# Kernel optimization log

Measured on AMD Instinct MI355X. Metric: run time of the kernel, lower is better.

Reference implementation:

```python
import jax, jax.numpy as jnp
import numpy as np

L, B, T, F, C, H, DFF = 2, 4, 2048, 1024, 200, 8, 128


def setup_inputs() -> dict:
    key = jax.random.key(0)
    ks = jax.random.split(key, 12)
    s = 0.02
    return {
        "x": jax.random.normal(ks[0], (B, T, F), jnp.float32),
        "prototypes": jax.random.normal(ks[1], (C, 1, F), jnp.float32),
        # conv_query / conv_key (1x1 convs == linear), per RAB layer
        "wq": jax.random.normal(ks[2], (L, F, F), jnp.float32) * s,
        "bq": jnp.zeros((L, F), jnp.float32),
        "wk": jax.random.normal(ks[3], (L, F, F), jnp.float32) * s,
        "bk": jnp.zeros((L, F), jnp.float32),
        # nn.MultiheadAttention packed in-proj and out-proj
        "in_w": jax.random.normal(ks[4], (L, 3 * F, F), jnp.float32) * s,
        "in_b": jnp.zeros((L, 3 * F), jnp.float32),
        "out_w": jax.random.normal(ks[5], (L, F, F), jnp.float32) * s,
        "out_b": jnp.zeros((L, F), jnp.float32),
        # FFN
        "l1_w": jax.random.normal(ks[6], (L, DFF, F), jnp.float32) * s,
        "l1_b": jnp.zeros((L, DFF), jnp.float32),
        "l2_w": jax.random.normal(ks[7], (L, F, DFF), jnp.float32) * s,
        "l2_b": jnp.zeros((L, F), jnp.float32),
        # LayerNorms
        "ln1_g": jnp.ones((L, F), jnp.float32),
        "ln1_b": jnp.zeros((L, F), jnp.float32),
        "ln2_g": jnp.ones((L, F), jnp.float32),
        "ln2_b": jnp.zeros((L, F), jnp.float32),
        # feature_embedding: Conv1d(F, F, k=3, pad=1) + ReLU
        "emb_w": jax.random.normal(ks[8], (F, F, 3), jnp.float32) * s,
        "emb_b": jnp.zeros((F,), jnp.float32),
    }


def _ln(x, g, b, eps=1e-5):
    mu = jnp.mean(x, axis=-1, keepdims=True)
    var = jnp.mean((x - mu) ** 2, axis=-1, keepdims=True)
    return (x - mu) * jax.lax.rsqrt(var + eps) * g + b


def _mha(q, k, v, w, b, ow, ob):
    # q,k,v: (B,S,F). Packed in-proj like nn.MultiheadAttention (eval: no dropout).
    f = q.shape[-1]
    dh = f // H
    Q = q @ w[:f].T + b[:f]
    K = k @ w[f:2 * f].T + b[f:2 * f]
    V = v @ w[2 * f:].T + b[2 * f:]
    sp = lambda t: t.reshape(t.shape[0], t.shape[1], H, dh)
    scale = np.float32(1.0 / np.sqrt(dh))
    att = jnp.einsum('bqhd,bkhd->bhqk', sp(Q), sp(K)) * scale
    att = jax.nn.softmax(att, axis=-1)
    o = jnp.einsum('bhqk,bkhd->bqhd', att, sp(V)).reshape(q.shape)
    return o @ ow.T + ob


def reference(x, prototypes, wq, bq, wk, bk, in_w, in_b, out_w, out_b,
              l1_w, l1_b, l2_w, l2_b, ln1_g, ln1_b, ln2_g, ln2_b, emb_w, emb_b):
    Bn, Tn, Fn = x.shape
    # torch: prototypes.view(1, F, -1)  (a reshape, NOT a transpose)
    proto = jnp.broadcast_to(prototypes.reshape(1, Fn, -1), (Bn, Fn, prototypes.shape[0]))
    # concat along time: (B,F,S) with S = T + C, then work in (B,S,F)
    src = jnp.swapaxes(jnp.concatenate([jnp.swapaxes(x, 1, 2), proto], axis=2), 1, 2)
    for l in range(L):
        q = src @ wq[l].T + bq[l]          # conv1x1 == pointwise linear
        k = src @ wk[l].T + bk[l]
        a = _mha(q, k, src, in_w[l], in_b[l], out_w[l], out_b[l])
        src = _ln(src + a, ln1_g[l], ln1_b[l])
        ff = jax.nn.relu(src @ l1_w[l].T + l1_b[l]) @ l2_w[l].T + l2_b[l]
        src = _ln(src + ff, ln2_g[l], ln2_b[l])
    feat = jnp.swapaxes(src[:, :Tn], 1, 2)  # (B,F,T): drop prototype tokens
    y = jax.lax.conv_general_dilated(feat, emb_w, (1,), ((1, 1),),
                                     dimension_numbers=('NCH', 'OIH', 'NCH'))
    return jax.nn.relu(y + emb_b[None, :, None])
```

## Files before the change

### kernel.cpp

```cpp
#include <hip/hip_runtime.h>
#include <hip/hip_bf16.h>


constexpr int BN = 4, TN = 2048, FD = 1024, CP = 200, SN = TN + CP;
constexpr int HN = 8, DH = 128, DF = 128, MR = BN * SN;
constexpr int SF = 3 * FD;
constexpr int NT = (SN + 63) / 64;
constexpr float C2 = 0.12751744f;

typedef __attribute__((ext_vector_type(8))) short short8;
typedef __attribute__((ext_vector_type(4))) float f32x4;

__device__ __forceinline__ ushort f2b(float f) {
  union { float f; uint u; } v{f};
  return (ushort)((v.u + 0x7fffu + ((v.u >> 16) & 1u)) >> 16);
}
__device__ __forceinline__ float b2f(ushort u) {
  union { uint u; float f; } v{(uint)u << 16};
  return v.f;
}
__device__ __forceinline__ uint cvt_pk_bf16(float a, float b) {
  uint r;
  asm("v_cvt_pk_bf16_f32 %0, %1, %2" : "=v"(r) : "v"(a), "v"(b));
  return r;
}
__device__ __forceinline__ float exp2_fast(float x) {
  float r;
  asm("v_exp_f32 %0, %1" : "=v"(r) : "v"(x));
  return r;
}
__device__ __forceinline__ void gld16(const void* g, void* l) {
  __builtin_amdgcn_global_load_lds(
      (const __attribute__((address_space(1))) void*)g,
      (__attribute__((address_space(3))) void*)l, 16, 0, 0);
}

__global__ __launch_bounds__(256) void k_build(const float* __restrict__ x,
                                               const float* __restrict__ proto,
                                               ushort* __restrict__ srcb) {
  const int row = blockIdx.x;
  const int b = row / SN, s = row % SN;
  const int f = threadIdx.x * 4;
  const size_t o = (size_t)row * FD + f;
  float4 v;
  if (s < TN) {
    v = *(const float4*)(x + ((size_t)b * TN + s) * FD + f);
  } else {
    const int c = s - TN;
    v.x = proto[(size_t)(f + 0) * CP + c];
    v.y = proto[(size_t)(f + 1) * CP + c];
    v.z = proto[(size_t)(f + 2) * CP + c];
    v.w = proto[(size_t)(f + 3) * CP + c];
  }
  ushort4 u{f2b(v.x), f2b(v.y), f2b(v.z), f2b(v.w)};
  *(ushort4*)(srcb + o) = u;
}

__global__ __launch_bounds__(256) void k_cvt(const float* __restrict__ in,
                                             ushort* __restrict__ out, int n) {
  const int n4 = n >> 2;
  for (int i = blockIdx.x * 256 + threadIdx.x; i < n4; i += gridDim.x * 256) {
    const float4 v = *(const float4*)(in + (size_t)i * 4);
    ushort4 u{f2b(v.x), f2b(v.y), f2b(v.z), f2b(v.w)};
    *(ushort4*)(out + (size_t)i * 4) = u;
  }
}

__global__ __launch_bounds__(256) void k_cvtT(const float* __restrict__ Wg,
                                              ushort* __restrict__ WTg) {
  const float* W = Wg + (size_t)blockIdx.z * FD * FD;
  ushort* WT = WTg + (size_t)blockIdx.z * FD * FD;
  __shared__ float t[32][33];
  const int tx = threadIdx.x & 31, ty = threadIdx.x >> 5;
  const int x0 = blockIdx.x * 32, y0 = blockIdx.y * 32;
#pragma unroll
  for (int dy = 0; dy < 4; ++dy)
    t[ty + dy * 8][tx] = W[(size_t)(y0 + ty + dy * 8) * FD + x0 + tx];
  __syncthreads();
#pragma unroll
  for (int dy = 0; dy < 4; ++dy)
    WT[(size_t)(x0 + ty + dy * 8) * FD + y0 + tx] = f2b(t[tx][ty + dy * 8]);
}

__global__ __launch_bounds__(256) void k_vT(const ushort* __restrict__ V,
                                            ushort* __restrict__ Vt) {
  __shared__ ushort t[32][34];
  const int tx = threadIdx.x & 31, ty = threadIdx.x >> 5;
  const int s0 = blockIdx.x * 32, d0 = blockIdx.y * 32, bh = blockIdx.z;
  const int b = bh >> 3, h = bh & 7;
#pragma unroll
  for (int dy = 0; dy < 4; ++dy) {
    const int s = min(s0 + ty + dy * 8, SN - 1);
    t[ty + dy * 8][tx] = V[((size_t)b * SN + s) * SF + h * DH + d0 + tx];
  }
  __syncthreads();
#pragma unroll
  for (int dy = 0; dy < 4; ++dy) {
    const int s = s0 + tx;
    if (s < SN)
      Vt[((size_t)bh * DH + d0 + ty + dy * 8) * SN + s] = t[tx][ty + dy * 8];
  }
}

__global__ __launch_bounds__(256) void k_convw(const float* __restrict__ W,
                                               ushort* __restrict__ out) {
  const int n = FD * FD * 3;
  for (int idx = blockIdx.x * 256 + threadIdx.x; idx < n;
       idx += gridDim.x * 256) {
    const int o = idx / (FD * 3);
    const int rem = idx % (FD * 3);
    const int tau = rem >> 10, i = rem & 1023;
    out[idx] = f2b(W[(size_t)o * (FD * 3) + i * 3 + tau]);
  }
}

__global__ __launch_bounds__(256) void k_pad(const ushort* __restrict__ sb,
                                             ushort* __restrict__ pad) {
  const int r = blockIdx.x, b = blockIdx.y;
  const int f = threadIdx.x * 4;
  ushort4 v{0, 0, 0, 0};
  if (r >= 1 && r <= TN)
    v = *(const ushort4*)(sb + ((size_t)b * SN + (r - 1)) * FD + f);
  *(ushort4*)(pad + ((size_t)b * (TN + 2) + r) * FD + f) = v;
}

__global__ __launch_bounds__(256) void k_beff(const float* __restrict__ in_w,
                                              const float* __restrict__ bvec,
                                              const float* __restrict__ in_b,
                                              float* __restrict__ out, int qk) {
  const int n = blockIdx.x, l = blockIdx.y, tid = threadIdx.x;
  const float* Win = in_w + (size_t)(l * 3 + qk) * FD * FD;
  const float* bv = bvec + (size_t)l * FD;
  float s = 0.f;
  for (int j = tid; j < FD; j += 256) s += Win[(size_t)n * FD + j] * bv[j];
  __shared__ float red[4];
#pragma unroll
  for (int o = 32; o; o >>= 1) s += __shfl_xor(s, o);
  if ((tid & 63) == 0) red[tid >> 6] = s;
  __syncthreads();
  if (tid == 0)
    out[l * 3 * FD + qk * FD + n] =
        red[0] + red[1] + red[2] + red[3] + in_b[l * 3 * FD + qk * FD + n];
}

__global__ __launch_bounds__(256) void k_copyv(const float* __restrict__ in_b,
                                               float* __restrict__ bqkv) {
  const int l = blockIdx.y;
  const int i = blockIdx.x * 256 + threadIdx.x;
  bqkv[l * 3 * FD + 2 * FD + i] = in_b[l * 3 * FD + 2 * FD + i];
}

template <bool RELU, bool BF16OUT>
__global__ __launch_bounds__(256) void k_mm(const ushort* __restrict__ A,
                                            const ushort* __restrict__ W,
                                            const float* __restrict__ bias,
                                            void* __restrict__ Cv,
                                            int M, int N, int K) {
  __shared__ __align__(16) ushort As[128 * 32];
  __shared__ __align__(16) ushort Ws[128 * 32];
  const int tid = threadIdx.x;
  const int lane = tid & 63, wv = tid >> 6;
  const int l15 = lane & 15, g = lane >> 4;
  const int wr = wv >> 1, wc = wv & 1;
  int bx = blockIdx.x, by = blockIdx.y;
  const int nwg = gridDim.x * gridDim.y;
  if ((nwg & 7) == 0) {
    int bid = by * gridDim.x + bx;
    bid = (bid & 7) * (nwg >> 3) + (bid >> 3);
    bx = bid % gridDim.x;
    by = bid / gridDim.x;
  }
  const int m0 = by * 128, n0 = bx * 128;
  f32x4 acc[4][4];
#pragma unroll
  for (int i = 0; i < 4; ++i)
#pragma unroll
    for (int j = 0; j < 4; ++j) acc[i][j] = (f32x4){0.f, 0.f, 0.f, 0.f};

  for (int k0 = 0; k0 < K; k0 += 32) {
#pragma unroll
    for (int j = 0; j < 2; ++j) {
      const int u = j * 256 + wv * 64 + lane;
      const int r = u >> 2, c = (u & 3) * 8;
      const int gm = min(m0 + r, M - 1);
      gld16(A + (size_t)gm * K + k0 + c, As + (size_t)u * 8);
    }
#pragma unroll
    for (int j = 0; j < 2; ++j) {
      const int u = j * 256 + wv * 64 + lane;
      const int r = u >> 2, c = (u & 3) * 8;
      gld16(W + (size_t)(n0 + r) * K + k0 + c, Ws + (size_t)u * 8);
    }
    __syncthreads();
    short8 af[4], bfr[4];
#pragma unroll
    for (int i = 0; i < 4; ++i)
      af[i] = *(const short8*)(As + (wr * 64 + i * 16 + l15) * 32 + g * 8);
#pragma unroll
    for (int j = 0; j < 4; ++j)
      bfr[j] = *(const short8*)(Ws + (wc * 64 + j * 16 + l15) * 32 + g * 8);
    __builtin_amdgcn_s_setprio(1);
#pragma unroll
    for (int i = 0; i < 4; ++i)
#pragma unroll
      for (int j = 0; j < 4; ++j)
        acc[i][j] = __builtin_amdgcn_mfma_f32_16x16x32_bf16(af[i], bfr[j],
                                                            acc[i][j], 0, 0, 0);
    __builtin_amdgcn_s_setprio(0);
    __syncthreads();
  }
#pragma unroll
  for (int i = 0; i < 4; ++i) {
#pragma unroll
    for (int r = 0; r < 4; ++r) {
      const int row = m0 + wr * 64 + i * 16 + g * 4 + r;
      if (row >= M) continue;
#pragma unroll
      for (int j = 0; j < 4; ++j) {
        const int col = n0 + wc * 64 + j * 16 + l15;
        float v = acc[i][j][r];
        if (bias) v += bias[col];
        if (RELU) v = fmaxf(v, 0.f);
        if (BF16OUT)
          ((ushort*)Cv)[(size_t)row * N + col] = f2b(v);
        else
          ((float*)Cv)[(size_t)row * N + col] = v;
      }
    }
  }
}

__global__ __launch_bounds__(256) void k_mmconv(const ushort* __restrict__ Ap,
                                                const ushort* __restrict__ W,
                                                const float* __restrict__ bias,
                                                float* __restrict__ Y) {
  constexpr int K = 3 * FD;
  __shared__ __align__(16) ushort As[128 * 32];
  __shared__ __align__(16) ushort Ws[128 * 32];
  const int tid = threadIdx.x;
  const int lane = tid & 63, wv = tid >> 6;
  const int l15 = lane & 15, g = lane >> 4;
  const int wr = wv >> 1, wc = wv & 1;
  int bx = blockIdx.x, by = blockIdx.y;
  const int nwg = gridDim.x * gridDim.y;
  if ((nwg & 7) == 0) {
    int bid = by * gridDim.x + bx;
    bid = (bid & 7) * (nwg >> 3) + (bid >> 3);
    bx = bid % gridDim.x;
    by = bid / gridDim.x;
  }
  const int m0 = by * 128, n0 = bx * 128;
  f32x4 acc[4][4];
#pragma unroll
  for (int i = 0; i < 4; ++i)
#pragma unroll
    for (int j = 0; j < 4; ++j) acc[i][j] = (f32x4){0.f, 0.f, 0.f, 0.f};

  for (int k0 = 0; k0 < K; k0 += 32) {
    const int tau = k0 >> 10;
    const int i0 = k0 & 1023;
#pragma unroll
    for (int j = 0; j < 2; ++j) {
      const int u = j * 256 + wv * 64 + lane;
      const int r = u >> 2, c = (u & 3) * 8;
      const int rm = m0 + r;
      const int b = rm >> 11, t = rm & 2047;
      gld16(Ap + ((size_t)(b * (TN + 2) + t + tau) * FD + i0 + c),
            As + (size_t)u * 8);
    }
#pragma unroll
    for (int j = 0; j < 2; ++j) {
      const int u = j * 256 + wv * 64 + lane;
      const int r = u >> 2, c = (u & 3) * 8;
      gld16(W + (size_t)(n0 + r) * K + k0 + c, Ws + (size_t)u * 8);
    }
    __syncthreads();
    short8 af[4], bfr[4];
#pragma unroll
    for (int i = 0; i < 4; ++i)
      af[i] = *(const short8*)(As + (wr * 64 + i * 16 + l15) * 32 + g * 8);
#pragma unroll
    for (int j = 0; j < 4; ++j)
      bfr[j] = *(const short8*)(Ws + (wc * 64 + j * 16 + l15) * 32 + g * 8);
    __builtin_amdgcn_s_setprio(1);
#pragma unroll
    for (int i = 0; i < 4; ++i)
#pragma unroll
      for (int j = 0; j < 4; ++j)
        acc[i][j] = __builtin_amdgcn_mfma_f32_16x16x32_bf16(af[i], bfr[j],
                                                            acc[i][j], 0, 0, 0);
    __builtin_amdgcn_s_setprio(0);
    __syncthreads();
  }
#pragma unroll
  for (int i = 0; i < 4; ++i) {
#pragma unroll
    for (int r = 0; r < 4; ++r) {
      const int rm = m0 + wr * 64 + i * 16 + g * 4 + r;
      const int b = rm >> 11, t = rm & 2047;
#pragma unroll
      for (int j = 0; j < 4; ++j) {
        const int col = n0 + wc * 64 + j * 16 + l15;
        const float v = fmaxf(acc[i][j][r] + bias[col], 0.f);
        Y[((size_t)(b * FD + col)) * TN + t] = v;
      }
    }
  }
}

__global__ __launch_bounds__(256) void k_fattn(const ushort* __restrict__ Qg,
                                               const ushort* __restrict__ Kg,
                                               const ushort* __restrict__ Vt,
                                               ushort* __restrict__ Og) {
  __shared__ __align__(16) ushort Ks[2][64 * 128];
  __shared__ __align__(16) ushort Vs[2][128 * 64];
  __shared__ __align__(16) ushort Ps[4][16 * 64];
  const int tid = threadIdx.x, lane = tid & 63, wv = tid >> 6;
  const int l15 = lane & 15, g = lane >> 4;
  const int b = blockIdx.z, h = blockIdx.y, q0 = blockIdx.x * 64;
  const size_t rowBase = (size_t)b * SN;
  const int hoff = h * DH;
  const size_t vbase = (size_t)(b * HN + h) * DH * SN;

  short8 qf[4];
  const int qrow = min(q0 + wv * 16 + l15, SN - 1);
#pragma unroll
  for (int c = 0; c < 4; ++c)
    qf[c] = *(const short8*)(Qg + (rowBase + qrow) * SF + hoff + c * 32 + g * 8);
  asm volatile("s_waitcnt vmcnt(0)" ::: "memory");

  short8 onesf;
#pragma unroll
  for (int i = 0; i < 8; ++i) onesf[i] = (short)0x3F80;

  f32x4 o[8];
#pragma unroll
  for (int dt = 0; dt < 8; ++dt) o[dt] = (f32x4){0.f, 0.f, 0.f, 0.f};
  f32x4 lacc = (f32x4){0.f, 0.f, 0.f, 0.f};
  char* PsB = (char*)&Ps[wv][0];

  auto stageK = [&](int kv0, ushort* dst, bool tail) {
#pragma unroll
    for (int j = 0; j < 4; ++j) {
      const int su = j * 256 + wv * 64 + lane;
      const int row = su >> 4, s = su & 15;
      const int c16 = s ^ (row & 7);
      const int krow = tail ? min(kv0 + row, SN - 1) : kv0 + row;
      gld16(Kg + (rowBase + krow) * SF + hoff + c16 * 8, dst + (size_t)su * 8);
    }
  };
  auto stageV = [&](int kv0, ushort* dst, bool tail) {
#pragma unroll
    for (int j = 0; j < 4; ++j) {
      const int su = j * 256 + wv * 64 + lane;
      const int row = su >> 3, s = su & 7;
      const int cc = s ^ (row & 7);
      const int kvc = tail ? min(kv0 + cc * 8, SN - 8) : kv0 + cc * 8;
      gld16(Vt + vbase + (size_t)row * SN + kvc, dst + (size_t)su * 8);
    }
  };

  stageK(0, Ks[0], false);
  stageV(0, Vs[0], false);

  for (int t = 0; t < NT; ++t) {
    const int kv0 = t * 64;
    const int cur = t & 1;
    if (t + 1 < NT) {
      const bool tl = (t + 1 == NT - 1);
      stageK(kv0 + 64, Ks[cur ^ 1], tl);
      stageV(kv0 + 64, Vs[cur ^ 1], tl);
      asm volatile("s_waitcnt vmcnt(8)" ::: "memory");
    } else {
      asm volatile("s_waitcnt vmcnt(0)" ::: "memory");
    }
    __builtin_amdgcn_s_barrier();
    __builtin_amdgcn_sched_barrier(0);
    const char* KsB = (const char*)Ks[cur];
    const char* VsB = (const char*)Vs[cur];

    f32x4 st[4];
    __builtin_amdgcn_s_setprio(1);
#pragma unroll
    for (int kt = 0; kt < 4; ++kt) {
      f32x4 s4 = (f32x4){0.f, 0.f, 0.f, 0.f};
      const int row = kt * 16 + l15;
#pragma unroll
      for (int c = 0; c < 4; ++c) {
        const short8 kf = *(const short8*)(
            KsB + row * 256 + (((c * 4 + g) ^ (row & 7)) << 4));
        s4 = __builtin_amdgcn_mfma_f32_16x16x32_bf16(kf, qf[c], s4, 0, 0, 0);
      }
      st[kt] = s4;
    }
    __builtin_amdgcn_s_setprio(0);

    float pfl[16];
    if (t == NT - 1) {
#pragma unroll
      for (int kt = 0; kt < 4; ++kt)
#pragma unroll
        for (int r = 0; r < 4; ++r) {
          const int kvg = kv0 + kt * 16 + g * 4 + r;
          pfl[kt * 4 + r] =
              (kvg < SN) ? exp2_fast(C2 * st[kt][r]) : 0.f;
        }
    } else {
#pragma unroll
      for (int i = 0; i < 16; ++i)
        pfl[i] = exp2_fast(C2 * st[i >> 2][i & 3]);
    }

#pragma unroll
    for (int kt = 0; kt < 4; ++kt) {
      const uint lo = cvt_pk_bf16(pfl[kt * 4 + 0], pfl[kt * 4 + 1]);
      const uint hi = cvt_pk_bf16(pfl[kt * 4 + 2], pfl[kt * 4 + 3]);
      const int slot = (kt * 2 + (g >> 1)) ^ (l15 & 7);
      *(uint2*)(PsB + l15 * 128 + slot * 16 + (g & 1) * 8) = make_uint2(lo, hi);
    }

    __builtin_amdgcn_s_setprio(1);
#pragma unroll
    for (int c2 = 0; c2 < 2; ++c2) {
      const int pslot = (c2 * 4 + g) ^ (l15 & 7);
      const short8 pf = *(const short8*)(PsB + l15 * 128 + pslot * 16);
      lacc = __builtin_amdgcn_mfma_f32_16x16x32_bf16(pf, onesf, lacc, 0, 0, 0);
#pragma unroll
      for (int dt = 0; dt < 8; ++dt) {
        const int row = dt * 16 + l15;
        const short8 vf = *(const short8*)(
            VsB + row * 128 + (((c2 * 4 + g) ^ (row & 7)) << 4));
        o[dt] = __builtin_amdgcn_mfma_f32_16x16x32_bf16(pf, vf, o[dt], 0, 0, 0);
      }
    }
    __builtin_amdgcn_s_setprio(0);
    __builtin_amdgcn_s_barrier();
  }

  float ir[4];
#pragma unroll
  for (int r = 0; r < 4; ++r) ir[r] = 1.f / lacc[r];
#pragma unroll
  for (int r = 0; r < 4; ++r) {
    const int orow = q0 + wv * 16 + g * 4 + r;
    if (orow >= SN) continue;
#pragma unroll
    for (int dt = 0; dt < 8; ++dt)
      Og[(rowBase + orow) * FD + hoff + dt * 16 + l15] = f2b(o[dt][r] * ir[r]);
  }
}

__global__ __launch_bounds__(256) void k_add_ln(ushort* __restrict__ sb,
                                                const ushort* __restrict__ d,
                                                const float* __restrict__ g,
                                                const float* __restrict__ be) {
  __shared__ float red[4];
  const int row = blockIdx.x;
  const int tid = threadIdx.x;
  const int c = tid * 4;
  const size_t off = (size_t)row * FD + c;
  const ushort4 sv = *(const ushort4*)(sb + off);
  const ushort4 dv = *(const ushort4*)(d + off);
  float v[4] = {b2f(sv.x) + b2f(dv.x), b2f(sv.y) + b2f(dv.y),
                b2f(sv.z) + b2f(dv.z), b2f(sv.w) + b2f(dv.w)};
  float sum = v[0] + v[1] + v[2] + v[3];
#pragma unroll
  for (int o = 32; o; o >>= 1) sum += __shfl_xor(sum, o);
  if ((tid & 63) == 0) red[tid >> 6] = sum;
  __syncthreads();
  sum = red[0] + red[1] + red[2] + red[3];
  const float mu = sum * (1.f / FD);
  float vs = 0.f;
#pragma unroll
  for (int i = 0; i < 4; ++i) {
    const float t = v[i] - mu;
    vs += t * t;
  }
  __syncthreads();
#pragma unroll
  for (int o = 32; o; o >>= 1) vs += __shfl_xor(vs, o);
  if ((tid & 63) == 0) red[tid >> 6] = vs;
  __syncthreads();
  vs = red[0] + red[1] + red[2] + red[3];
  const float rstd = rsqrtf(vs * (1.f / FD) + 1e-5f);
  const float4 gv = *(const float4*)(g + c);
  const float4 bv = *(const float4*)(be + c);
  ushort4 u{f2b((v[0] - mu) * rstd * gv.x + bv.x),
            f2b((v[1] - mu) * rstd * gv.y + bv.y),
            f2b((v[2] - mu) * rstd * gv.z + bv.z),
            f2b((v[3] - mu) * rstd * gv.w + bv.w)};
  *(ushort4*)(sb + off) = u;
}

extern "C" void kernel_launch(void* const* d_in, const int* in_sizes, int n_in,
                              void* d_out, int out_size, void* d_ws,
                              size_t ws_size, hipStream_t stream) {
  const float* x      = (const float*)d_in[0];
  const float* proto  = (const float*)d_in[1];
  const float* wq     = (const float*)d_in[2];
  const float* bq     = (const float*)d_in[3];
  const float* wk     = (const float*)d_in[4];
  const float* bk     = (const float*)d_in[5];
  const float* in_w   = (const float*)d_in[6];
  const float* in_b   = (const float*)d_in[7];
  const float* out_w  = (const float*)d_in[8];
  const float* out_b  = (const float*)d_in[9];
  const float* l1_w   = (const float*)d_in[10];
  const float* l1_b   = (const float*)d_in[11];
  const float* l2_w   = (const float*)d_in[12];
  const float* l2_b   = (const float*)d_in[13];
  const float* ln1_g  = (const float*)d_in[14];
  const float* ln1_b  = (const float*)d_in[15];
  const float* ln2_g  = (const float*)d_in[16];
  const float* ln2_b  = (const float*)d_in[17];
  const float* emb_w  = (const float*)d_in[18];
  const float* emb_b  = (const float*)d_in[19];

  char* p = (char*)d_ws;
  auto take = [&](size_t bytes) {
    char* r = p;
    p += (bytes + 255) & ~(size_t)255;
    return r;
  };
  const size_t MF = (size_t)MR * FD;
  const size_t FF = (size_t)FD * FD;
  ushort* srcb  = (ushort*)take(MF * 2);
  ushort* bQKV  = (ushort*)take((size_t)MR * SF * 2);
  ushort* bVt   = (ushort*)take((size_t)BN * HN * DH * SN * 2);
  ushort* bO    = (ushort*)take(MF * 2);
  ushort* bFF   = (ushort*)take((size_t)MR * DF * 2);
  ushort* wQKV  = (ushort*)take((size_t)2 * 3 * FF * 2);
  ushort* wOut  = (ushort*)take((size_t)2 * FF * 2);
  ushort* wL1   = (ushort*)take((size_t)2 * DF * FD * 2);
  ushort* wL2   = (ushort*)take((size_t)2 * FD * DF * 2);
  float*  bqkv  = (float*)take((size_t)2 * SF * 4);
  ushort* wT     = bQKV;
  ushort* wInQK  = bQKV + 4 * FF;
  ushort* bOut   = bQKV;
  ushort* srcPad = bQKV;
  ushort* convW  = bQKV + (size_t)10 * 1024 * 1024;

  k_build<<<MR, 256, 0, stream>>>(x, proto, srcb);
  k_cvt<<<1024, 256, 0, stream>>>(in_w, wInQK, 2 * FF);
  k_cvt<<<1024, 256, 0, stream>>>(in_w + 3 * FF, wInQK + 2 * FF, 2 * FF);
  k_cvt<<<1024, 256, 0, stream>>>(in_w + 2 * FF, wQKV + 2 * FF, FF);
  k_cvt<<<1024, 256, 0, stream>>>(in_w + 5 * FF, wQKV + 5 * FF, FF);
  k_cvt<<<1024, 256, 0, stream>>>(out_w, wOut, 2 * FF);
  k_cvt<<<256, 256, 0, stream>>>(l1_w, wL1, 2 * DF * FD);
  k_cvt<<<256, 256, 0, stream>>>(l2_w, wL2, 2 * FD * DF);
  k_cvtT<<<dim3(32, 32, 2), 256, 0, stream>>>(wq, wT);
  k_cvtT<<<dim3(32, 32, 2), 256, 0, stream>>>(wk, wT + 2 * FF);
  for (int l = 0; l < 2; ++l)
    for (int qk = 0; qk < 2; ++qk)
      k_mm<false, true><<<dim3(8, 8), 256, 0, stream>>>(
          wInQK + (size_t)(l * 2 + qk) * FF, wT + (size_t)(qk * 2 + l) * FF,
          nullptr, wQKV + (size_t)(l * 3 + qk) * FF, FD, FD, FD);
  k_beff<<<dim3(FD, 2), 256, 0, stream>>>(in_w, bq, in_b, bqkv, 0);
  k_beff<<<dim3(FD, 2), 256, 0, stream>>>(in_w, bk, in_b, bqkv, 1);
  k_copyv<<<dim3(4, 2), 256, 0, stream>>>(in_b, bqkv);

  for (int l = 0; l < 2; ++l) {
    k_mm<false, true><<<dim3(SF / 128, (MR + 127) / 128), 256, 0, stream>>>(
        srcb, wQKV + (size_t)l * 3 * FF, bqkv + (size_t)l * SF, bQKV, MR, SF,
        FD);
    k_vT<<<dim3((SN + 31) / 32, DH / 32, BN * HN), 256, 0, stream>>>(
        bQKV + 2 * FD, bVt);
    k_fattn<<<dim3((SN + 63) / 64, HN, BN), 256, 0, stream>>>(
        bQKV, bQKV + FD, bVt, bO);
    k_mm<false, true><<<dim3(FD / 128, (MR + 127) / 128), 256, 0, stream>>>(
        bO, wOut + (size_t)l * FF, out_b + (size_t)l * FD, bOut, MR, FD, FD);
    k_add_ln<<<MR, 256, 0, stream>>>(srcb, bOut, ln1_g + (size_t)l * FD,
                                     ln1_b + (size_t)l * FD);
    k_mm<true, true><<<dim3(DF / 128, (MR + 127) / 128), 256, 0, stream>>>(
        srcb, wL1 + (size_t)l * DF * FD, l1_b + (size_t)l * DF, bFF, MR, DF,
        FD);
    k_mm<false, true><<<dim3(FD / 128, (MR + 127) / 128), 256, 0, stream>>>(
        bFF, wL2 + (size_t)l * FD * DF, l2_b + (size_t)l * FD, bOut, MR, FD,
        DF);
    k_add_ln<<<MR, 256, 0, stream>>>(srcb, bOut, ln2_g + (size_t)l * FD,
                                     ln2_b + (size_t)l * FD);
  }

  k_convw<<<1024, 256, 0, stream>>>(emb_w, convW);
  k_pad<<<dim3(TN + 2, BN), 256, 0, stream>>>(srcb, srcPad);
  k_mmconv<<<dim3(FD / 128, (BN * TN) / 128), 256, 0, stream>>>(
      srcPad, convW, emb_b, (float*)d_out);
}
```

Measured before the change: 1.067 ms.

## Add double-buffered 128x256 GEMM kernel and single-buffer attention K/V staging

Introduces a templated 512-thread GEMM with 128x256 tiles, K-step 64, XOR-swizzled LDS and double-buffered async global-to-LDS prefetch. It replaces the QKV projection, the output projection and the conv-as-GEMM kernels, aiming for more operand reuse per tile and overlap of loads with MFMA work. Separately, the flash-attention kernel drops its K/V double buffering in favour of a single buffer with full syncthreads, cutting LDS use to allow more resident blocks but losing load/compute overlap within a block. The GEMM also clamps rows beyond M instead of predicating, and uses launch_bounds(512,1), which may limit occupancy.

After: 1.049 ms. About the same (-1.7%).

```diff
diff --git a/kernel.cpp b/kernel.cpp
--- a/kernel.cpp
+++ b/kernel.cpp
@@ -230,17 +230,18 @@
   }
 }
 
-__global__ __launch_bounds__(256) void k_mmconv(const ushort* __restrict__ Ap,
+template <bool CONV, bool BF16OUT>
+__global__ __launch_bounds__(512, 1) void k_mmB(const ushort* __restrict__ A,
                                                 const ushort* __restrict__ W,
                                                 const float* __restrict__ bias,
-                                                float* __restrict__ Y) {
-  constexpr int K = 3 * FD;
-  __shared__ __align__(16) ushort As[128 * 32];
-  __shared__ __align__(16) ushort Ws[128 * 32];
+                                                void* __restrict__ Cv,
+                                                int M, int N, int K) {
+  __shared__ __align__(16) ushort As[2][128 * 64];
+  __shared__ __align__(16) ushort Bs[2][256 * 64];
   const int tid = threadIdx.x;
   const int lane = tid & 63, wv = tid >> 6;
   const int l15 = lane & 15, g = lane >> 4;
-  const int wr = wv >> 1, wc = wv & 1;
+  const int wr = wv >> 2, wc = wv & 3;
   int bx = blockIdx.x, by = blockIdx.y;
   const int nwg = gridDim.x * gridDim.y;
   if ((nwg & 7) == 0) {
@@ -249,60 +250,101 @@
     bx = bid % gridDim.x;
     by = bid / gridDim.x;
   }
-  const int m0 = by * 128, n0 = bx * 128;
+  const int m0 = by * 128, n0 = bx * 256;
+  const int NKt = K >> 6;
+
   f32x4 acc[4][4];
 #pragma unroll
   for (int i = 0; i < 4; ++i)
 #pragma unroll
     for (int j = 0; j < 4; ++j) acc[i][j] = (f32x4){0.f, 0.f, 0.f, 0.f};
 
-  for (int k0 = 0; k0 < K; k0 += 32) {
-    const int tau = k0 >> 10;
-    const int i0 = k0 & 1023;
+  auto stage = [&](int kt, int d) {
+    const int kb = kt * 64;
 #pragma unroll
     for (int j = 0; j < 2; ++j) {
-      const int u = j * 256 + wv * 64 + lane;
-      const int r = u >> 2, c = (u & 3) * 8;
-      const int rm = m0 + r;
-      const int b = rm >> 11, t = rm & 2047;
-      gld16(Ap + ((size_t)(b * (TN + 2) + t + tau) * FD + i0 + c),
-            As + (size_t)u * 8);
-    }
-#pragma unroll
-    for (int j = 0; j < 2; ++j) {
-      const int u = j * 256 + wv * 64 + lane;
-      const int r = u >> 2, c = (u & 3) * 8;
-      gld16(W + (size_t)(n0 + r) * K + k0 + c, Ws + (size_t)u * 8);
-    }
-    __syncthreads();
-    short8 af[4], bfr[4];
-#pragma unroll
-    for (int i = 0; i < 4; ++i)
-      af[i] = *(const short8*)(As + (wr * 64 + i * 16 + l15) * 32 + g * 8);
-#pragma unroll
-    for (int j = 0; j < 4; ++j)
-      bfr[j] = *(const short8*)(Ws + (wc * 64 + j * 16 + l15) * 32 + g * 8);
-    __builtin_amdgcn_s_setprio(1);
-#pragma unroll
-    for (int i = 0; i < 4; ++i)
-#pragma unroll
-      for (int j = 0; j < 4; ++j)
-        acc[i][j] = __builtin_amdgcn_mfma_f32_16x16x32_bf16(af[i], bfr[j],
-                                                            acc[i][j], 0, 0, 0);
-    __builtin_amdgcn_s_setprio(0);
-    __syncthreads();
-  }
-#pragma unroll
-  for (int i = 0; i < 4; ++i) {
+      const int u = j * 512 + tid;
+      const int row = u >> 3, s = u & 7;
+      const int c = s ^ (row & 7);
+      const ushort* ga;
+      if (CONV) {
+        const int rm = m0 + row;
+        const int bb = rm >> 11, tt = rm & 2047;
+        ga = A + (size_t)(bb * (TN + 2) + tt + (kb >> 10)) * FD + (kb & 1023) +
+             c * 8;
+      } else {
+        ga = A + (size_t)min(m0 + row, M - 1) * K + kb + c * 8;
+      }
+      gld16(ga, As[d] + row * 64 + s * 8);
+    }
+#pragma unroll
+    for (int j = 0; j < 4; ++j) {
+      const int u = j * 512 + tid;
+      const int row = u >> 3, s = u & 7;
+      const int c = s ^ (row & 7);
+      gld16(W + (size_t)(n0 + row) * K + kb + c * 8, Bs[d] + row * 64 + s * 8);
+    }
+  };
+
+  stage(0, 0);
+  for (int kt = 0; kt < NKt; ++kt) {
+    const int cur = kt & 1;
+    if (kt + 1 < NKt) {
+      stage(kt + 1, cur ^ 1);
+      asm volatile("s_waitcnt vmcnt(6)" ::: "memory");
+    } else {
+      asm volatile("s_waitcnt vmcnt(0)" ::: "memory");
+    }
+    __builtin_amdgcn_s_barrier();
+    __builtin_amdgcn_sched_barrier(0);
+#pragma unroll
+    for (int ks = 0; ks < 2; ++ks) {
+      short8 aq[4], bq[4];
+#pragma unroll
+      for (int mf = 0; mf < 4; ++mf) {
+        const int row = wr * 64 + mf * 16 + l15;
+        aq[mf] = *(const short8*)(As[cur] + row * 64 +
+                                  (((ks * 4 + g) ^ (row & 7)) << 3));
+      }
+#pragma unroll
+      for (int nf = 0; nf < 4; ++nf) {
+        const int row = wc * 64 + nf * 16 + l15;
+        bq[nf] = *(const short8*)(Bs[cur] + row * 64 +
+                                  (((ks * 4 + g) ^ (row & 7)) << 3));
+      }
+      __builtin_amdgcn_s_setprio(1);
+#pragma unroll
+      for (int mf = 0; mf < 4; ++mf)
+#pragma unroll
+        for (int nf = 0; nf < 4; ++nf)
+          acc[mf][nf] = __builtin_amdgcn_mfma_f32_16x16x32_bf16(
+              aq[mf], bq[nf], acc[mf][nf], 0, 0, 0);
+      __builtin_amdgcn_s_setprio(0);
+    }
+    asm volatile("s_waitcnt lgkmcnt(0)" ::: "memory");
+    __builtin_amdgcn_s_barrier();
+  }
+
+#pragma unroll
+  for (int mf = 0; mf < 4; ++mf) {
 #pragma unroll
     for (int r = 0; r < 4; ++r) {
-      const int rm = m0 + wr * 64 + i * 16 + g * 4 + r;
-      const int b = rm >> 11, t = rm & 2047;
-#pragma unroll
-      for (int j = 0; j < 4; ++j) {
-        const int col = n0 + wc * 64 + j * 16 + l15;
-        const float v = fmaxf(acc[i][j][r] + bias[col], 0.f);
-        Y[((size_t)(b * FD + col)) * TN + t] = v;
+      const int row = m0 + wr * 64 + mf * 16 + g * 4 + r;
+      if (!CONV && row >= M) continue;
+#pragma unroll
+      for (int nf = 0; nf < 4; ++nf) {
+        const int col = n0 + wc * 64 + nf * 16 + l15;
+        float v = acc[mf][nf][r];
+        if (bias) v += bias[col];
+        if (CONV) {
+          v = fmaxf(v, 0.f);
+          const int bb = row >> 11, tt = row & 2047;
+          ((float*)Cv)[((size_t)(bb * FD + col)) * TN + tt] = v;
+        } else if (BF16OUT) {
+          ((ushort*)Cv)[(size_t)row * N + col] = f2b(v);
+        } else {
+          ((float*)Cv)[(size_t)row * N + col] = v;
+        }
       }
     }
   }
@@ -312,8 +354,8 @@
                                                const ushort* __restrict__ Kg,
                                                const ushort* __restrict__ Vt,
                                                ushort* __restrict__ Og) {
-  __shared__ __align__(16) ushort Ks[2][64 * 128];
-  __shared__ __align__(16) ushort Vs[2][128 * 64];
+  __shared__ __align__(16) ushort Ks[64 * 128];
+  __shared__ __align__(16) ushort Vs[128 * 64];
   __shared__ __align__(16) ushort Ps[4][16 * 64];
   const int tid = threadIdx.x, lane = tid & 63, wv = tid >> 6;
   const int l15 = lane & 15, g = lane >> 4;
@@ -327,7 +369,6 @@
 #pragma unroll
   for (int c = 0; c < 4; ++c)
     qf[c] = *(const short8*)(Qg + (rowBase + qrow) * SF + hoff + c * 32 + g * 8);
-  asm volatile("s_waitcnt vmcnt(0)" ::: "memory");
 
   short8 onesf;
 #pragma unroll
@@ -337,47 +378,49 @@
 #pragma unroll
   for (int dt = 0; dt < 8; ++dt) o[dt] = (f32x4){0.f, 0.f, 0.f, 0.f};
   f32x4 lacc = (f32x4){0.f, 0.f, 0.f, 0.f};
+  const char* KsB = (const char*)Ks;
+  const char* VsB = (const char*)Vs;
   char* PsB = (char*)&Ps[wv][0];
-
-  auto stageK = [&](int kv0, ushort* dst, bool tail) {
-#pragma unroll
-    for (int j = 0; j < 4; ++j) {
-      const int su = j * 256 + wv * 64 + lane;
-      const int row = su >> 4, s = su & 15;
-      const int c16 = s ^ (row & 7);
-      const int krow = tail ? min(kv0 + row, SN - 1) : kv0 + row;
-      gld16(Kg + (rowBase + krow) * SF + hoff + c16 * 8, dst + (size_t)su * 8);
-    }
-  };
-  auto stageV = [&](int kv0, ushort* dst, bool tail) {
-#pragma unroll
-    for (int j = 0; j < 4; ++j) {
-      const int su = j * 256 + wv * 64 + lane;
-      const int row = su >> 3, s = su & 7;
-      const int cc = s ^ (row & 7);
-      const int kvc = tail ? min(kv0 + cc * 8, SN - 8) : kv0 + cc * 8;
-      gld16(Vt + vbase + (size_t)row * SN + kvc, dst + (size_t)su * 8);
-    }
-  };
-
-  stageK(0, Ks[0], false);
-  stageV(0, Vs[0], false);
 
   for (int t = 0; t < NT; ++t) {
     const int kv0 = t * 64;
-    const int cur = t & 1;
-    if (t + 1 < NT) {
-      const bool tl = (t + 1 == NT - 1);
-      stageK(kv0 + 64, Ks[cur ^ 1], tl);
-      stageV(kv0 + 64, Vs[cur ^ 1], tl);
-      asm volatile("s_waitcnt vmcnt(8)" ::: "memory");
+    const bool tl = (t == NT - 1);
+    if (tl) {
+#pragma unroll
+      for (int j = 0; j < 4; ++j) {
+        const int su = j * 256 + tid;
+        const int row = su >> 4, s = su & 15;
+        const int c16 = s ^ (row & 7);
+        const int krow = min(kv0 + row, SN - 1);
+        gld16(Kg + (rowBase + krow) * SF + hoff + c16 * 8, Ks + (size_t)su * 8);
+      }
+#pragma unroll
+      for (int j = 0; j < 4; ++j) {
+        const int su = j * 256 + tid;
+        const int row = su >> 3, s = su & 7;
+        const int cc = s ^ (row & 7);
+        const int kvc = min(kv0 + cc * 8, SN - 8);
+        gld16(Vt + vbase + (size_t)row * SN + kvc, Vs + (size_t)su * 8);
+      }
     } else {
-      asm volatile("s_waitcnt vmcnt(0)" ::: "memory");
-    }
-    __builtin_amdgcn_s_barrier();
-    __builtin_amdgcn_sched_barrier(0);
-    const char* KsB = (const char*)Ks[cur];
-    const char* VsB = (const char*)Vs[cur];
+#pragma unroll
+      for (int j = 0; j < 4; ++j) {
+        const int su = j * 256 + tid;
+        const int row = su >> 4, s = su & 15;
+        const int c16 = s ^ (row & 7);
+        gld16(Kg + (rowBase + kv0 + row) * SF + hoff + c16 * 8,
+              Ks + (size_t)su * 8);
+      }
+#pragma unroll
+      for (int j = 0; j < 4; ++j) {
+        const int su = j * 256 + tid;
+        const int row = su >> 3, s = su & 7;
+        const int cc = s ^ (row & 7);
+        gld16(Vt + vbase + (size_t)row * SN + kv0 + cc * 8,
+              Vs + (size_t)su * 8);
+      }
+    }
+    __syncthreads();
 
     f32x4 st[4];
     __builtin_amdgcn_s_setprio(1);
@@ -396,14 +439,13 @@
     __builtin_amdgcn_s_setprio(0);
 
     float pfl[16];
-    if (t == NT - 1) {
+    if (tl) {
 #pragma unroll
       for (int kt = 0; kt < 4; ++kt)
 #pragma unroll
         for (int r = 0; r < 4; ++r) {
           const int kvg = kv0 + kt * 16 + g * 4 + r;
-          pfl[kt * 4 + r] =
-              (kvg < SN) ? exp2_fast(C2 * st[kt][r]) : 0.f;
+          pfl[kt * 4 + r] = (kvg < SN) ? exp2_fast(C2 * st[kt][r]) : 0.f;
         }
     } else {
 #pragma unroll
@@ -434,7 +476,7 @@
       }
     }
     __builtin_amdgcn_s_setprio(0);
-    __builtin_amdgcn_s_barrier();
+    __syncthreads();
   }
 
   float ir[4];
@@ -559,22 +601,24 @@
   k_beff<<<dim3(FD, 2), 256, 0, stream>>>(in_w, bk, in_b, bqkv, 1);
   k_copyv<<<dim3(4, 2), 256, 0, stream>>>(in_b, bqkv);
 
+  const int MB = (MR + 127) / 128;
+
   for (int l = 0; l < 2; ++l) {
-    k_mm<false, true><<<dim3(SF / 128, (MR + 127) / 128), 256, 0, stream>>>(
+    k_mmB<false, true><<<dim3(SF / 256, MB), 512, 0, stream>>>(
         srcb, wQKV + (size_t)l * 3 * FF, bqkv + (size_t)l * SF, bQKV, MR, SF,
         FD);
     k_vT<<<dim3((SN + 31) / 32, DH / 32, BN * HN), 256, 0, stream>>>(
         bQKV + 2 * FD, bVt);
     k_fattn<<<dim3((SN + 63) / 64, HN, BN), 256, 0, stream>>>(
         bQKV, bQKV + FD, bVt, bO);
-    k_mm<false, true><<<dim3(FD / 128, (MR + 127) / 128), 256, 0, stream>>>(
+    k_mmB<false, true><<<dim3(FD / 256, MB), 512, 0, stream>>>(
         bO, wOut + (size_t)l * FF, out_b + (size_t)l * FD, bOut, MR, FD, FD);
     k_add_ln<<<MR, 256, 0, stream>>>(srcb, bOut, ln1_g + (size_t)l * FD,
                                      ln1_b + (size_t)l * FD);
-    k_mm<true, true><<<dim3(DF / 128, (MR + 127) / 128), 256, 0, stream>>>(
+    k_mm<true, true><<<dim3(DF / 128, MB), 256, 0, stream>>>(
         srcb, wL1 + (size_t)l * DF * FD, l1_b + (size_t)l * DF, bFF, MR, DF,
         FD);
-    k_mm<false, true><<<dim3(FD / 128, (MR + 127) / 128), 256, 0, stream>>>(
+    k_mm<false, true><<<dim3(FD / 128, MB), 256, 0, stream>>>(
         bFF, wL2 + (size_t)l * FD * DF, l2_b + (size_t)l * FD, bOut, MR, FD,
         DF);
     k_add_ln<<<MR, 256, 0, stream>>>(srcb, bOut, ln2_g + (size_t)l * FD,
@@ -583,6 +627,6 @@
 
   k_convw<<<1024, 256, 0, stream>>>(emb_w, convW);
   k_pad<<<dim3(TN + 2, BN), 256, 0, stream>>>(srcb, srcPad);
-  k_mmconv<<<dim3(FD / 128, (BN * TN) / 128), 256, 0, stream>>>(
-      srcPad, convW, emb_b, (float*)d_out);
-}
+  k_mmB<true, false><<<dim3(FD / 256, (BN * TN) / 128), 512, 0, stream>>>(
+      srcPad, convW, emb_b, (float*)d_out, BN * TN, FD, 3 * FD);
+}
```
